# Performance work log

Measured on AMD Instinct MI355X. Metric: run time of the kernel, lower is better.

## Reference

```python
import jax, jax.numpy as jnp
import numpy as np

B, S, D, F, E = 4, 2048, 2048, 4096, 8


def setup_inputs() -> dict:
    key = jax.random.key(0)
    k1, k2, k3, k4 = jax.random.split(key, 4)
    hidden_states = jax.random.normal(k1, (B, S, D), dtype=jnp.float32)
    router_logits = jax.random.normal(k2, (B, S, E), dtype=jnp.float32)
    # per-expert FFN weights, scaled for stable magnitudes
    w1 = jax.random.normal(k3, (E, F, D), dtype=jnp.float32) / np.sqrt(D)
    w2 = jax.random.normal(k4, (E, D, F), dtype=jnp.float32) / np.sqrt(F)
    return {"hidden_states": hidden_states, "router_logits": router_logits, "w1": w1, "w2": w2}


def reference(hidden_states, router_logits, w1, w2):
    # Top-1 routing: each token goes to exactly one expert (argmax of logits).
    b, s, d = hidden_states.shape
    e = w1.shape[0]
    x = hidden_states.reshape(-1, d)                 # [T, D], T = B*S
    assign = jnp.argmax(router_logits.reshape(-1, e), axis=-1)  # [T] int
    out = jnp.zeros_like(x)
    # Fixed small loop over experts (structurally distinct weights);
    # each iteration: dense GEMM -> SiLU -> dense GEMM, masked combine.
    for ei in range(e):
        h = jax.nn.silu(x @ w1[ei].T) @ w2[ei].T     # [T, D]
        out = out + jnp.where((assign == ei)[:, None], h, 0.0)
    return out.reshape(b, s, d)
```

## Files before the change

kernel.cpp:

```cpp
#include <hip/hip_runtime.h>
#include <stdint.h>

#define T_TOKENS 8192
#define DDIM 2048
#define FDIM 4096
#define NEXP 8
#define MAXTILES 72

typedef __attribute__((ext_vector_type(8))) short bf16x8;
typedef __attribute__((ext_vector_type(4))) float f32x4;

__device__ __forceinline__ unsigned short f2bf(float f) {
  unsigned int u = __float_as_uint(f);
  unsigned int r = (u + 0x7FFFu + ((u >> 16) & 1u)) >> 16;
  return (unsigned short)r;
}

__global__ void k_assign(const float* __restrict__ logits,
                         int* __restrict__ assign,
                         int* __restrict__ counts) {
  int t = blockIdx.x * blockDim.x + threadIdx.x;
  if (t >= T_TOKENS) return;
  const float* l = logits + (size_t)t * NEXP;
  float bv = l[0]; int be = 0;
#pragma unroll
  for (int e = 1; e < NEXP; ++e) {
    float v = l[e];
    if (v > bv) { bv = v; be = e; }
  }
  assign[t] = be;
  atomicAdd(&counts[be], 1);
}

__global__ void k_scan(const int* __restrict__ counts,
                       int* __restrict__ offsets,
                       int* __restrict__ tile_e,
                       int* __restrict__ tile_rb,
                       int* __restrict__ ntiles) {
  if (threadIdx.x == 0) {
    int acc = 0, nt = 0;
    for (int e = 0; e < NEXP; ++e) {
      offsets[e] = acc;
      int c = counts[e];
      acc += c;
      int t = (c + 127) >> 7;
      for (int i = 0; i < t; ++i) { tile_e[nt] = e; tile_rb[nt] = i; ++nt; }
    }
    ntiles[0] = nt;
  }
}

__global__ void k_place(const int* __restrict__ assign,
                        const int* __restrict__ offsets,
                        int* __restrict__ cursors,
                        int* __restrict__ perm) {
  int t = blockIdx.x * blockDim.x + threadIdx.x;
  if (t >= T_TOKENS) return;
  int e = assign[t];
  int pos = atomicAdd(&cursors[e], 1);
  perm[offsets[e] + pos] = t;
}

__global__ void k_gather_x(const float* __restrict__ x,
                           const int* __restrict__ perm,
                           unsigned short* __restrict__ xg) {
  const int total = T_TOKENS * (DDIM / 4);
  const int stride = gridDim.x * blockDim.x;
  for (int idx = blockIdx.x * blockDim.x + threadIdx.x; idx < total; idx += stride) {
    int slot = idx / (DDIM / 4);
    int c4 = idx - slot * (DDIM / 4);
    int tok = perm[slot];
    float4 v = ((const float4*)(x + (size_t)tok * DDIM))[c4];
    ushort4 o;
    o.x = f2bf(v.x); o.y = f2bf(v.y); o.z = f2bf(v.z); o.w = f2bf(v.w);
    ((ushort4*)(xg + (size_t)slot * DDIM))[c4] = o;
  }
}

__global__ void k_cast2(const float* __restrict__ s1, const float* __restrict__ s2,
                        unsigned short* __restrict__ d1, unsigned short* __restrict__ d2,
                        int n4) {
  const int stride = gridDim.x * blockDim.x;
  for (int i = blockIdx.x * blockDim.x + threadIdx.x; i < 2 * n4; i += stride) {
    float4 v;
    if (i < n4) v = ((const float4*)s1)[i];
    else        v = ((const float4*)s2)[i - n4];
    ushort4 o;
    o.x = f2bf(v.x); o.y = f2bf(v.y); o.z = f2bf(v.z); o.w = f2bf(v.w);
    if (i < n4) ((ushort4*)d1)[i] = o;
    else        ((ushort4*)d2)[i - n4] = o;
  }
}

__device__ __forceinline__ void glds(const unsigned short* g, unsigned short* l) {
  __builtin_amdgcn_global_load_lds(
      (const __attribute__((address_space(1))) void*)g,
      (__attribute__((address_space(3))) void*)l, 16, 0, 0);
}

template<bool FIRST>
__launch_bounds__(512, 4)
__global__ void k_gemm(const unsigned short* __restrict__ Ap,
                       const unsigned short* __restrict__ Bw,
                       unsigned short* __restrict__ Hout,
                       float* __restrict__ Out,
                       const int* __restrict__ offsets,
                       const int* __restrict__ counts,
                       const int* __restrict__ perm,
                       const int* __restrict__ tile_e,
                       const int* __restrict__ tile_rb,
                       const int* __restrict__ ntiles) {
  constexpr int K   = FIRST ? DDIM : FDIM;
  constexpr int N   = FIRST ? FDIM : DDIM;
  constexpr int NS  = K / 32;
  constexpr int ASL = 128 * 32;
  constexpr int BSL = 256 * 32;

  const int ty = blockIdx.y;
  if (ty >= ntiles[0]) return;
  const int e   = tile_e[ty];
  const int rb  = tile_rb[ty] << 7;
  const int off = offsets[e];
  const int Me  = counts[e];
  const int cb  = blockIdx.x << 8;

  extern __shared__ unsigned short sm[];
  unsigned short* At = sm;
  unsigned short* Bt = sm + 3 * ASL;

  const int tid  = threadIdx.x;
  const int wave = tid >> 6;
  const int lane = tid & 63;
  const int wr   = wave >> 2;
  const int wc   = wave & 3;

  const int tq  = tid >> 2;
  const int kd8 = (((tid & 3) ^ ((tid >> 3) & 3)) << 3);

  int ar = rb + tq; if (ar >= Me) ar = Me - 1;
  const unsigned short* gA  = Ap + (size_t)(off + ar) * K + kd8;
  const unsigned short* gB0 = Bw + (size_t)e * N * K + (size_t)(cb + tq) * K + kd8;
  const unsigned short* gB1 = gB0 + (size_t)128 * K;

  const int dlo = wave * 512;

#pragma unroll
  for (int s = 0; s < 2; ++s) {
    glds(gA  + s * 32, At + s * ASL + dlo);
    glds(gB0 + s * 32, Bt + s * BSL + dlo);
    glds(gB1 + s * 32, Bt + s * BSL + dlo + 128 * 32);
  }
  asm volatile("s_waitcnt vmcnt(3)" ::: "memory");
  __builtin_amdgcn_s_barrier();
  asm volatile("" ::: "memory");

  const int kswz8 = (((lane >> 4) ^ ((lane >> 1) & 3)) << 3);
  const int aoff  = (wr * 64 + (lane & 15)) * 32 + kswz8;
  const int boff  = (wc * 64 + (lane & 15)) * 32 + kswz8;

  f32x4 acc[4][4] = {};
  int cur = 0, pre = 2;
  for (int ks = 0; ks < NS; ++ks) {
    int ka = ks + 2; if (ka >= NS) ka -= NS;
    const int ko = ka * 32;
    const unsigned short* Ac = At + cur * ASL + aoff;
    const unsigned short* Bc = Bt + cur * BSL + boff;

    bf16x8 af[4], bf[4];
#pragma unroll
    for (int m = 0; m < 4; ++m) af[m] = *(const bf16x8*)(Ac + m * 512);
#pragma unroll
    for (int n = 0; n < 4; ++n) bf[n] = *(const bf16x8*)(Bc + n * 512);

    glds(gA  + ko, At + pre * ASL + dlo);
    glds(gB0 + ko, Bt + pre * BSL + dlo);
    glds(gB1 + ko, Bt + pre * BSL + dlo + 128 * 32);

    asm volatile("s_waitcnt vmcnt(3)" ::: "memory");
    __builtin_amdgcn_s_barrier();
    asm volatile("s_waitcnt lgkmcnt(0)" ::: "memory");
    __builtin_amdgcn_sched_barrier(0);
    __builtin_amdgcn_s_setprio(1);
#pragma unroll
    for (int m = 0; m < 4; ++m)
#pragma unroll
      for (int n = 0; n < 4; ++n)
        acc[m][n] = __builtin_amdgcn_mfma_f32_16x16x32_bf16(af[m], bf[n], acc[m][n], 0, 0, 0);
    __builtin_amdgcn_s_setprio(0);
    __builtin_amdgcn_s_barrier();

    cur = (cur == 2) ? 0 : cur + 1;
    pre = (pre == 2) ? 0 : pre + 1;
  }

  const int ccol = lane & 15;
  const int cr0 = (lane >> 4) * 4;
  const int colbase = cb + wc * 64;
#pragma unroll
  for (int i = 0; i < 4; ++i) {
#pragma unroll
    for (int r = 0; r < 4; ++r) {
      int row = rb + wr * 64 + i * 16 + cr0 + r;
      if (row < Me) {
        if constexpr (FIRST) {
          unsigned short* hrow = Hout + (size_t)(off + row) * N;
#pragma unroll
          for (int j = 0; j < 4; ++j) {
            float v = acc[i][j][r];
            float s = v / (1.0f + __expf(-v));
            hrow[colbase + j * 16 + ccol] = f2bf(s);
          }
        } else {
          int tok = perm[off + row];
          float* orow = Out + (size_t)tok * N;
#pragma unroll
          for (int j = 0; j < 4; ++j)
            orow[colbase + j * 16 + ccol] = acc[i][j][r];
        }
      }
    }
  }
}

extern "C" void kernel_launch(void* const* d_in, const int* in_sizes, int n_in,
                              void* d_out, int out_size, void* d_ws, size_t ws_size,
                              hipStream_t stream) {
  const float* x      = (const float*)d_in[0];
  const float* logits = (const float*)d_in[1];
  const float* w1     = (const float*)d_in[2];
  const float* w2     = (const float*)d_in[3];
  float* out = (float*)d_out;

  char* ws = (char*)d_ws;
  int* counts  = (int*)(ws + 0);
  int* offsets = (int*)(ws + 64);
  int* cursors = (int*)(ws + 128);
  int* tile_e  = (int*)(ws + 256);
  int* tile_rb = (int*)(ws + 1024);
  int* ntiles  = (int*)(ws + 2048);
  int* assign  = (int*)(ws + 4096);
  int* perm    = (int*)(ws + 4096 + T_TOKENS * 4);
  size_t p = 4096 + (size_t)2 * T_TOKENS * 4;
  p = (p + 255) & ~(size_t)255;
  unsigned short* Xg  = (unsigned short*)(ws + p); p += (size_t)T_TOKENS * DDIM * 2;
  unsigned short* W1b = (unsigned short*)(ws + p); p += (size_t)NEXP * FDIM * DDIM * 2;
  unsigned short* W2b = (unsigned short*)(ws + p); p += (size_t)NEXP * DDIM * FDIM * 2;
  unsigned short* Hb  = (unsigned short*)(ws + p); p += (size_t)T_TOKENS * FDIM * 2;
  if (ws_size < p) return;

  hipFuncSetAttribute(reinterpret_cast<const void*>(k_gemm<true>),
                      hipFuncAttributeMaxDynamicSharedMemorySize, 73728);
  hipFuncSetAttribute(reinterpret_cast<const void*>(k_gemm<false>),
                      hipFuncAttributeMaxDynamicSharedMemorySize, 73728);

  hipMemsetAsync(ws, 0, 4096, stream);
  k_assign<<<T_TOKENS / 256, 256, 0, stream>>>(logits, assign, counts);
  k_scan<<<1, 64, 0, stream>>>(counts, offsets, tile_e, tile_rb, ntiles);
  k_place<<<T_TOKENS / 256, 256, 0, stream>>>(assign, offsets, cursors, perm);
  k_gather_x<<<2048, 256, 0, stream>>>(x, perm, Xg);
  int n4 = NEXP * FDIM * (DDIM / 4);
  k_cast2<<<2048, 256, 0, stream>>>(w1, w2, W1b, W2b, n4);
  k_gemm<true><<<dim3(FDIM / 256, MAXTILES), 512, 73728, stream>>>(
      Xg, W1b, Hb, nullptr, offsets, counts, perm, tile_e, tile_rb, ntiles);
  k_gemm<false><<<dim3(DDIM / 256, MAXTILES), 512, 73728, stream>>>(
      Hb, W2b, nullptr, out, offsets, counts, perm, tile_e, tile_rb, ntiles);
}
```

Before: 1.068 ms.

## Restructure GEMM to 4 waves with 128x64 per-wave tiles, fuse place+gather

The grouped GEMM moves from 512 threads in a 2x4 wave grid to 256 threads. Each wave now computes a 128x64 output sub-tile with 32 accumulators, using a double buffer in static LDS instead of a triple buffer in dynamic LDS. Each wave gets more MFMA work per fragment load, which cuts LDS read traffic per FLOP. The cost is more registers, fewer waves per CU and an extra barrier per k-step. Token placement and the bf16 gather of x are also fused into one kernel with one block per token, which removes a launch and the perm indirection on reads.

Measured after the change: 1.145 ms. 7.2% more time.

```diff
diff --git a/kernel.cpp b/kernel.cpp
--- a/kernel.cpp
+++ b/kernel.cpp
@@ -50,30 +50,32 @@
   }
 }
 
-__global__ void k_place(const int* __restrict__ assign,
-                        const int* __restrict__ offsets,
-                        int* __restrict__ cursors,
-                        int* __restrict__ perm) {
-  int t = blockIdx.x * blockDim.x + threadIdx.x;
-  if (t >= T_TOKENS) return;
-  int e = assign[t];
-  int pos = atomicAdd(&cursors[e], 1);
-  perm[offsets[e] + pos] = t;
-}
-
-__global__ void k_gather_x(const float* __restrict__ x,
-                           const int* __restrict__ perm,
-                           unsigned short* __restrict__ xg) {
-  const int total = T_TOKENS * (DDIM / 4);
-  const int stride = gridDim.x * blockDim.x;
-  for (int idx = blockIdx.x * blockDim.x + threadIdx.x; idx < total; idx += stride) {
-    int slot = idx / (DDIM / 4);
-    int c4 = idx - slot * (DDIM / 4);
-    int tok = perm[slot];
-    float4 v = ((const float4*)(x + (size_t)tok * DDIM))[c4];
+__global__ void k_place_gather(const float* __restrict__ x,
+                               const int* __restrict__ assign,
+                               const int* __restrict__ offsets,
+                               int* __restrict__ cursors,
+                               int* __restrict__ perm,
+                               unsigned short* __restrict__ xg) {
+  const int t = blockIdx.x;
+  __shared__ int slot_s;
+  if (threadIdx.x == 0) {
+    int e = assign[t];
+    int pos = atomicAdd(&cursors[e], 1);
+    int slot = offsets[e] + pos;
+    perm[slot] = t;
+    slot_s = slot;
+  }
+  __syncthreads();
+  const int slot = slot_s;
+  const float4* src = (const float4*)(x + (size_t)t * DDIM);
+  ushort4* dst = (ushort4*)(xg + (size_t)slot * DDIM);
+#pragma unroll
+  for (int c = 0; c < 2; ++c) {
+    int c4 = threadIdx.x + c * 256;
+    float4 v = src[c4];
     ushort4 o;
     o.x = f2bf(v.x); o.y = f2bf(v.y); o.z = f2bf(v.z); o.w = f2bf(v.w);
-    ((ushort4*)(xg + (size_t)slot * DDIM))[c4] = o;
+    dst[c4] = o;
   }
 }
 
@@ -99,7 +101,7 @@
 }
 
 template<bool FIRST>
-__launch_bounds__(512, 4)
+__launch_bounds__(256, 2)
 __global__ void k_gemm(const unsigned short* __restrict__ Ap,
                        const unsigned short* __restrict__ Bw,
                        unsigned short* __restrict__ Hout,
@@ -110,11 +112,9 @@
                        const int* __restrict__ tile_e,
                        const int* __restrict__ tile_rb,
                        const int* __restrict__ ntiles) {
-  constexpr int K   = FIRST ? DDIM : FDIM;
-  constexpr int N   = FIRST ? FDIM : DDIM;
-  constexpr int NS  = K / 32;
-  constexpr int ASL = 128 * 32;
-  constexpr int BSL = 256 * 32;
+  constexpr int K  = FIRST ? DDIM : FDIM;
+  constexpr int N  = FIRST ? FDIM : DDIM;
+  constexpr int NS = K / 32;
 
   const int ty = blockIdx.y;
   if (ty >= ntiles[0]) return;
@@ -124,83 +124,80 @@
   const int Me  = counts[e];
   const int cb  = blockIdx.x << 8;
 
-  extern __shared__ unsigned short sm[];
-  unsigned short* At = sm;
-  unsigned short* Bt = sm + 3 * ASL;
+  __shared__ unsigned short At[2][128 * 32];
+  __shared__ unsigned short Bt[2][256 * 32];
 
   const int tid  = threadIdx.x;
   const int wave = tid >> 6;
   const int lane = tid & 63;
-  const int wr   = wave >> 2;
-  const int wc   = wave & 3;
-
-  const int tq  = tid >> 2;
+
+  const int tq4 = tid >> 2;
   const int kd8 = (((tid & 3) ^ ((tid >> 3) & 3)) << 3);
 
-  int ar = rb + tq; if (ar >= Me) ar = Me - 1;
-  const unsigned short* gA  = Ap + (size_t)(off + ar) * K + kd8;
-  const unsigned short* gB0 = Bw + (size_t)e * N * K + (size_t)(cb + tq) * K + kd8;
-  const unsigned short* gB1 = gB0 + (size_t)128 * K;
-
-  const int dlo = wave * 512;
+  int ar0 = rb + tq4;      if (ar0 >= Me) ar0 = Me - 1;
+  int ar1 = rb + 64 + tq4; if (ar1 >= Me) ar1 = Me - 1;
+  const unsigned short* gA0 = Ap + (size_t)(off + ar0) * K + kd8;
+  const unsigned short* gA1 = Ap + (size_t)(off + ar1) * K + kd8;
+  const unsigned short* gB  = Bw + (size_t)e * N * K + (size_t)(cb + tq4) * K + kd8;
+
+  const int dA = wave * 512;
 
 #pragma unroll
   for (int s = 0; s < 2; ++s) {
-    glds(gA  + s * 32, At + s * ASL + dlo);
-    glds(gB0 + s * 32, Bt + s * BSL + dlo);
-    glds(gB1 + s * 32, Bt + s * BSL + dlo + 128 * 32);
-  }
-  asm volatile("s_waitcnt vmcnt(3)" ::: "memory");
-  __builtin_amdgcn_s_barrier();
-  asm volatile("" ::: "memory");
+    glds(gA0 + s * 32, &At[s][dA]);
+    glds(gA1 + s * 32, &At[s][2048 + dA]);
+#pragma unroll
+    for (int t = 0; t < 4; ++t)
+      glds(gB + (size_t)t * 64 * K + s * 32, &Bt[s][t * 2048 + dA]);
+  }
 
   const int kswz8 = (((lane >> 4) ^ ((lane >> 1) & 3)) << 3);
-  const int aoff  = (wr * 64 + (lane & 15)) * 32 + kswz8;
-  const int boff  = (wc * 64 + (lane & 15)) * 32 + kswz8;
-
-  f32x4 acc[4][4] = {};
-  int cur = 0, pre = 2;
+  const int abase = (lane & 15) * 32 + kswz8;
+  const int bbase = wave * 2048 + (lane & 15) * 32 + kswz8;
+
+  f32x4 acc[8][4] = {};
+
   for (int ks = 0; ks < NS; ++ks) {
+    const int c = ks & 1;
     int ka = ks + 2; if (ka >= NS) ka -= NS;
     const int ko = ka * 32;
-    const unsigned short* Ac = At + cur * ASL + aoff;
-    const unsigned short* Bc = Bt + cur * BSL + boff;
-
-    bf16x8 af[4], bf[4];
-#pragma unroll
-    for (int m = 0; m < 4; ++m) af[m] = *(const bf16x8*)(Ac + m * 512);
-#pragma unroll
-    for (int n = 0; n < 4; ++n) bf[n] = *(const bf16x8*)(Bc + n * 512);
-
-    glds(gA  + ko, At + pre * ASL + dlo);
-    glds(gB0 + ko, Bt + pre * BSL + dlo);
-    glds(gB1 + ko, Bt + pre * BSL + dlo + 128 * 32);
-
-    asm volatile("s_waitcnt vmcnt(3)" ::: "memory");
+
+    asm volatile("s_waitcnt vmcnt(6)" ::: "memory");
     __builtin_amdgcn_s_barrier();
+
+    bf16x8 af[8], bf[4];
+#pragma unroll
+    for (int i = 0; i < 8; ++i) af[i] = *(const bf16x8*)&At[c][i * 512 + abase];
+#pragma unroll
+    for (int n = 0; n < 4; ++n) bf[n] = *(const bf16x8*)&Bt[c][n * 512 + bbase];
     asm volatile("s_waitcnt lgkmcnt(0)" ::: "memory");
     __builtin_amdgcn_sched_barrier(0);
+    __builtin_amdgcn_s_barrier();
+
+    glds(gA0 + ko, &At[c][dA]);
+    glds(gA1 + ko, &At[c][2048 + dA]);
+#pragma unroll
+    for (int t = 0; t < 4; ++t)
+      glds(gB + (size_t)t * 64 * K + ko, &Bt[c][t * 2048 + dA]);
+    __builtin_amdgcn_sched_barrier(0);
+
     __builtin_amdgcn_s_setprio(1);
 #pragma unroll
-    for (int m = 0; m < 4; ++m)
+    for (int i = 0; i < 8; ++i)
 #pragma unroll
       for (int n = 0; n < 4; ++n)
-        acc[m][n] = __builtin_amdgcn_mfma_f32_16x16x32_bf16(af[m], bf[n], acc[m][n], 0, 0, 0);
+        acc[i][n] = __builtin_amdgcn_mfma_f32_16x16x32_bf16(af[i], bf[n], acc[i][n], 0, 0, 0);
     __builtin_amdgcn_s_setprio(0);
-    __builtin_amdgcn_s_barrier();
-
-    cur = (cur == 2) ? 0 : cur + 1;
-    pre = (pre == 2) ? 0 : pre + 1;
   }
 
   const int ccol = lane & 15;
   const int cr0 = (lane >> 4) * 4;
-  const int colbase = cb + wc * 64;
-#pragma unroll
-  for (int i = 0; i < 4; ++i) {
+  const int colbase = cb + wave * 64;
+#pragma unroll
+  for (int i = 0; i < 8; ++i) {
 #pragma unroll
     for (int r = 0; r < 4; ++r) {
-      int row = rb + wr * 64 + i * 16 + cr0 + r;
+      int row = rb + i * 16 + cr0 + r;
       if (row < Me) {
         if constexpr (FIRST) {
           unsigned short* hrow = Hout + (size_t)(off + row) * N;
@@ -248,20 +245,14 @@
   unsigned short* Hb  = (unsigned short*)(ws + p); p += (size_t)T_TOKENS * FDIM * 2;
   if (ws_size < p) return;
 
-  hipFuncSetAttribute(reinterpret_cast<const void*>(k_gemm<true>),
-                      hipFuncAttributeMaxDynamicSharedMemorySize, 73728);
-  hipFuncSetAttribute(reinterpret_cast<const void*>(k_gemm<false>),
-                      hipFuncAttributeMaxDynamicSharedMemorySize, 73728);
-
   hipMemsetAsync(ws, 0, 4096, stream);
   k_assign<<<T_TOKENS / 256, 256, 0, stream>>>(logits, assign, counts);
   k_scan<<<1, 64, 0, stream>>>(counts, offsets, tile_e, tile_rb, ntiles);
-  k_place<<<T_TOKENS / 256, 256, 0, stream>>>(assign, offsets, cursors, perm);
-  k_gather_x<<<2048, 256, 0, stream>>>(x, perm, Xg);
+  k_place_gather<<<T_TOKENS, 256, 0, stream>>>(x, assign, offsets, cursors, perm, Xg);
   int n4 = NEXP * FDIM * (DDIM / 4);
   k_cast2<<<2048, 256, 0, stream>>>(w1, w2, W1b, W2b, n4);
-  k_gemm<true><<<dim3(FDIM / 256, MAXTILES), 512, 73728, stream>>>(
+  k_gemm<true><<<dim3(FDIM / 256, MAXTILES), 256, 0, stream>>>(
       Xg, W1b, Hb, nullptr, offsets, counts, perm, tile_e, tile_rb, ntiles);
-  k_gemm<false><<<dim3(DDIM / 256, MAXTILES), 512, 73728, stream>>>(
+  k_gemm<false><<<dim3(DDIM / 256, MAXTILES), 256, 0, stream>>>(
       Hb, W2b, nullptr, out, offsets, counts, perm, tile_e, tile_rb, ntiles);
 }
```
